# Kernel tuning notes

Hardware: AMD Instinct MI355X
Metric: run time of the kernel (lower is better)

Reference implementation:

```python
import jax, jax.numpy as jnp
import numpy as np

B, DIM, H, W = 1, 256, 64, 64
NUM_HEADS = 8
N_GROUPS = 4
KK = 9                      # ksizes[blk_ids=0]
KV_H, KV_W = 64, 64         # kv_size[blk_ids=0]
NGC = DIM // N_GROUPS       # n_group_channels = 64
NHC = DIM // NUM_HEADS      # n_head_channels = 32
NGH = NUM_HEADS // N_GROUPS # n_group_heads = 2
OFFSET_RANGE_FACTOR = 2.0
SCALE = NHC ** -0.5
LN_EPS = 1e-5


def setup_inputs() -> dict:
    key = jax.random.key(0)
    ks = jax.random.split(key, 10)
    def n(k, shape, std=0.02):
        return jax.random.normal(k, shape, jnp.float32) * std
    return {
        "x": jax.random.normal(ks[0], (B, DIM, H, W), jnp.float32),
        "wq": n(ks[1], (DIM, DIM)), "bq": jnp.zeros((DIM,), jnp.float32),
        "wk": n(ks[2], (DIM, DIM)), "bk": jnp.zeros((DIM,), jnp.float32),
        "wv": n(ks[3], (DIM, DIM)), "bv": jnp.zeros((DIM,), jnp.float32),
        "w_off_dw": n(ks[4], (NGC, 1, KK, KK)), "b_off_dw": jnp.zeros((NGC,), jnp.float32),
        "ln_g": jnp.ones((NGC,), jnp.float32), "ln_b": jnp.zeros((NGC,), jnp.float32),
        "w_off_pw": n(ks[5], (2, NGC)),
        "rpe_table": n(ks[6], (NUM_HEADS, 2 * KV_H - 1, 2 * KV_W - 1), 0.01),
        "w_out": n(ks[7], (DIM, DIM)), "b_out": jnp.zeros((DIM,), jnp.float32),
    }


def conv1x1(x, w, b=None):
    # x: [B,C,H,W], w: [O,C]
    y = jnp.einsum('bchw,oc->bohw', x, w)
    if b is not None:
        y = y + b[None, :, None, None]
    return y


def grid_sample_bilinear(inp, grid):
    # Faithful F.grid_sample(mode='bilinear', align_corners=True, padding_mode='zeros').
    # inp: [N,C,Hi,Wi], grid: [N,Hg,Wg,2] with (x,y) in [-1,1].
    N, C, Hi, Wi = inp.shape
    gx = (grid[..., 0] + 1.0) * 0.5 * (Wi - 1)
    gy = (grid[..., 1] + 1.0) * 0.5 * (Hi - 1)
    x0 = jnp.floor(gx)
    y0 = jnp.floor(gy)
    gather_b = jax.vmap(lambda im, iy, ix: im[:, iy, ix])  # -> [N,C,Hg,Wg]
    out = jnp.zeros((N, C) + grid.shape[1:3], inp.dtype)
    for dy in (0.0, 1.0):
        for dx in (0.0, 1.0):
            ix = x0 + dx
            iy = y0 + dy
            wgt = (1.0 - jnp.abs(gx - ix)) * (1.0 - jnp.abs(gy - iy))
            valid = (ix >= 0) & (ix <= Wi - 1) & (iy >= 0) & (iy <= Hi - 1)
            ixc = jnp.clip(ix, 0, Wi - 1).astype(jnp.int32)
            iyc = jnp.clip(iy, 0, Hi - 1).astype(jnp.int32)
            out = out + gather_b(inp, iyc, ixc) * (wgt * valid)[:, None]
    return out


def ref_points(Hk, Wk, n):
    # normalized (y, x) reference grid, matching _get_ref_points
    ry = (jnp.arange(Hk, dtype=jnp.float32) + 0.5) / Hk * 2.0 - 1.0
    rx = (jnp.arange(Wk, dtype=jnp.float32) + 0.5) / Wk * 2.0 - 1.0
    ref = jnp.stack(jnp.meshgrid(ry, rx, indexing='ij'), -1)  # [Hk,Wk,2]
    return jnp.broadcast_to(ref[None], (n, Hk, Wk, 2))


def reference(x, wq, bq, wk, bk, wv, bv, w_off_dw, b_off_dw, ln_g, ln_b,
              w_off_pw, rpe_table, w_out, b_out):
    Bx, C, Hx, Wx = x.shape
    q = conv1x1(x, wq, bq)
    q_off = q.reshape(Bx * N_GROUPS, NGC, Hx, Wx)

    # conv_offset: depthwise conv -> LayerNorm(channels) -> GELU -> 1x1 conv (no bias)
    o = jax.lax.conv_general_dilated(
        q_off, w_off_dw, window_strides=(1, 1),
        padding=[(KK // 2, KK // 2), (KK // 2, KK // 2)],
        feature_group_count=NGC,
        dimension_numbers=('NCHW', 'OIHW', 'NCHW'))
    o = o + b_off_dw[None, :, None, None]
    mu = o.mean(1, keepdims=True)
    var = o.var(1, keepdims=True)
    o = (o - mu) / jnp.sqrt(var + LN_EPS) * ln_g[None, :, None, None] + ln_b[None, :, None, None]
    o = jax.nn.gelu(o, approximate=False)
    offset = jnp.einsum('bchw,oc->bohw', o, w_off_pw)  # [B*g, 2, Hk, Wk]

    Hk, Wk = offset.shape[2], offset.shape[3]
    n_sample = Hk * Wk
    off_range = jnp.array([1.0 / Hk, 1.0 / Wk], jnp.float32).reshape(1, 2, 1, 1)
    offset = jnp.tanh(offset) * off_range * OFFSET_RANGE_FACTOR
    offset = offset.transpose(0, 2, 3, 1)  # [B*g, Hk, Wk, 2] (y, x)

    pos = offset + ref_points(Hk, Wk, Bx * N_GROUPS)

    x_g = x.reshape(Bx * N_GROUPS, NGC, Hx, Wx)
    x_sampled = grid_sample_bilinear(x_g, pos[..., ::-1])  # grid is (x, y)
    x_sampled = x_sampled.reshape(Bx, C, 1, n_sample)

    qf = q.reshape(Bx * NUM_HEADS, NHC, Hx * Wx)
    k = conv1x1(x_sampled, wk, bk).reshape(Bx * NUM_HEADS, NHC, n_sample)
    v = conv1x1(x_sampled, wv, bv).reshape(Bx * NUM_HEADS, NHC, n_sample)

    attn = jnp.einsum('bcm,bcn->bmn', qf, k) * SCALE  # [B*h, HW, n_sample]

    # RPE bias via bilinear sampling of rpe_table at displacement grid
    q_grid = ref_points(Hx, Wx, Bx * N_GROUPS)
    disp = (q_grid.reshape(Bx * N_GROUPS, Hx * Wx, 1, 2)
            - pos.reshape(Bx * N_GROUPS, 1, n_sample, 2)) * 0.5
    rpe = jnp.broadcast_to(rpe_table[None], (Bx,) + rpe_table.shape)
    rpe = rpe.reshape(Bx * N_GROUPS, NGH, 2 * Hx - 1, 2 * Wx - 1)
    attn_bias = grid_sample_bilinear(rpe, disp[..., ::-1])
    attn_bias = attn_bias.reshape(Bx * NUM_HEADS, Hx * Wx, n_sample)

    attn = jax.nn.softmax(attn + attn_bias, axis=2)
    out = jnp.einsum('bmn,bcn->bcm', attn, v).reshape(Bx, C, Hx, Wx)
    return conv1x1(out, w_out, b_out)
```

## Files before the change

### kernel.cpp

```cpp
#include <hip/hip_runtime.h>
#include <hip/hip_bf16.h>
#include <math.h>

#define HW 4096
#define SCALE 0.17677669529663687f
#define LOG2E 1.4426950408889634f

typedef __attribute__((ext_vector_type(8))) short short8;
typedef __attribute__((ext_vector_type(4))) float f32x4;
typedef __attribute__((ext_vector_type(4))) unsigned int u32x4;
typedef __attribute__((ext_vector_type(2))) unsigned int u32x2;
typedef __attribute__((ext_vector_type(2), aligned(8))) unsigned int u32x2a;

static __device__ __forceinline__ unsigned short bf16b(float f) {
  __hip_bfloat16 h = __float2bfloat16(f);
  return *reinterpret_cast<unsigned short*>(&h);
}

__global__ __launch_bounds__(256) void gemm256(const float* __restrict__ W,
                                               const float* __restrict__ bias,
                                               const float* __restrict__ X,
                                               float* __restrict__ Yf,
                                               unsigned short* __restrict__ Yt,
                                               float sc) {
  int tid = threadIdx.x;
  int o0 = (blockIdx.x >> 4) * 8;
  int p = (blockIdx.x & 15) * 256 + tid;
  const float* Wb = W + o0 * 256;
  float acc[8];
  #pragma unroll
  for (int i = 0; i < 8; ++i) acc[i] = 0.f;
  #pragma unroll 4
  for (int c = 0; c < 256; ++c) {
    float xv = X[c * HW + p];
    #pragma unroll
    for (int i = 0; i < 8; ++i) acc[i] += Wb[i * 256 + c] * xv;
  }
  float r[8];
  #pragma unroll
  for (int i = 0; i < 8; ++i) r[i] = acc[i] + bias[o0 + i];
  if (Yf) {
    #pragma unroll
    for (int i = 0; i < 8; ++i) Yf[(size_t)(o0 + i) * HW + p] = r[i];
  }
  if (Yt) {
    int h = o0 >> 5, c0 = o0 & 31;
    u32x4 pk;
    #pragma unroll
    for (int j = 0; j < 4; ++j)
      pk[j] = (unsigned int)bf16b(r[2 * j] * sc) | ((unsigned int)bf16b(r[2 * j + 1] * sc) << 16);
    *(u32x4*)(Yt + ((size_t)(h * HW + p) * 32 + c0)) = pk;
  }
}

__global__ __launch_bounds__(256) void gemm_kv(const float* __restrict__ Wk,
                                               const float* __restrict__ bk,
                                               const float* __restrict__ Wv,
                                               const float* __restrict__ bv,
                                               const float* __restrict__ X,
                                               unsigned short* __restrict__ Yt,
                                               unsigned short* __restrict__ Yv) {
  int tid = threadIdx.x;
  int o0 = (blockIdx.x >> 4) * 8;
  int p = (blockIdx.x & 15) * 256 + tid;
  const float* Wkb = Wk + o0 * 256;
  const float* Wvb = Wv + o0 * 256;
  float ka[8], va[8];
  #pragma unroll
  for (int i = 0; i < 8; ++i) { ka[i] = 0.f; va[i] = 0.f; }
  #pragma unroll 2
  for (int c = 0; c < 256; ++c) {
    float xv = X[c * HW + p];
    #pragma unroll
    for (int i = 0; i < 8; ++i) {
      ka[i] += Wkb[i * 256 + c] * xv;
      va[i] += Wvb[i * 256 + c] * xv;
    }
  }
  {
    int h = o0 >> 5, c0 = o0 & 31;
    u32x4 pk;
    #pragma unroll
    for (int j = 0; j < 4; ++j) {
      float k0 = ka[2 * j] + bk[o0 + 2 * j];
      float k1 = ka[2 * j + 1] + bk[o0 + 2 * j + 1];
      pk[j] = (unsigned int)bf16b(k0) | ((unsigned int)bf16b(k1) << 16);
    }
    *(u32x4*)(Yt + ((size_t)(h * HW + p) * 32 + c0)) = pk;
  }
  #pragma unroll
  for (int i = 0; i < 8; ++i)
    Yv[(size_t)(o0 + i) * HW + p] = bf16b(va[i] + bv[o0 + i]);
}

__global__ __launch_bounds__(256) void dwconv_kernel(const float* __restrict__ q,
                                                     const float* __restrict__ wdw,
                                                     const float* __restrict__ bdw,
                                                     float* __restrict__ o) {
  int x = threadIdx.x & 63;
  int w = threadIdx.x >> 6;
  int bid = blockIdx.x;
  int half = bid & 1; int c = (bid >> 1) & 63; int g = bid >> 7;
  int y0 = half * 32 + w * 8;
  const float* qc = q + (g * 64 + c) * HW;
  const float* wc = wdw + c * 81;
  float b = bdw[c];
  float acc[8];
  #pragma unroll
  for (int i = 0; i < 8; ++i) acc[i] = b;
  #pragma unroll
  for (int r = 0; r < 16; ++r) {
    int yy = y0 - 4 + r;
    bool rowok = (unsigned)yy <= 63u;
    int yc = min(max(yy, 0), 63);
    float v[9];
    #pragma unroll
    for (int kx = 0; kx < 9; ++kx) {
      int xx = x + kx - 4;
      bool ok = rowok && ((unsigned)xx <= 63u);
      int xc = min(max(xx, 0), 63);
      float lv = qc[yc * 64 + xc];
      v[kx] = ok ? lv : 0.f;
    }
    #pragma unroll
    for (int oy = 0; oy < 8; ++oy) {
      int ky = r - oy;
      if (ky < 0 || ky > 8) continue;
      #pragma unroll
      for (int kx = 0; kx < 9; ++kx)
        acc[oy] += wc[ky * 9 + kx] * v[kx];
    }
  }
  #pragma unroll
  for (int oy = 0; oy < 8; ++oy)
    o[(g * 64 + c) * HW + (y0 + oy) * 64 + x] = acc[oy];
}

__global__ __launch_bounds__(256) void ln_offset_kernel(const float* __restrict__ o,
                                                        const float* __restrict__ ln_g,
                                                        const float* __restrict__ ln_b,
                                                        const float* __restrict__ wpw,
                                                        float* __restrict__ pos,
                                                        float* __restrict__ cxy) {
  int wave = threadIdx.x >> 6;
  int c = threadIdx.x & 63;
  int bid = blockIdx.x;
  int xc = bid & 15; int y = (bid >> 4) & 63; int g = bid >> 10;
  int x = xc * 4 + wave;
  int p = y * 64 + x;
  float v = o[(g * 64 + c) * HW + p];
  float s = v, s2 = v * v;
  #pragma unroll
  for (int m = 32; m; m >>= 1) { s += __shfl_xor(s, m); s2 += __shfl_xor(s2, m); }
  float mu = s * (1.f / 64.f);
  float var = s2 * (1.f / 64.f) - mu * mu;
  float nv = (v - mu) * rsqrtf(var + 1e-5f) * ln_g[c] + ln_b[c];
  nv = 0.5f * nv * (1.f + erff(nv * 0.70710678118654752f));
  float t0 = wpw[c] * nv, t1 = wpw[64 + c] * nv;
  #pragma unroll
  for (int m = 32; m; m >>= 1) { t0 += __shfl_xor(t0, m); t1 += __shfl_xor(t1, m); }
  if (c == 0) {
    float offy = tanhf(t0) * (2.0f / 64.0f);
    float offx = tanhf(t1) * (2.0f / 64.0f);
    float py = offy + (y + 0.5f) * (2.f / 64.f) - 1.f;
    float px = offx + (x + 0.5f) * (2.f / 64.f) - 1.f;
    pos[(g * HW + p) * 2 + 0] = py;
    pos[(g * HW + p) * 2 + 1] = px;
    cxy[(g * HW + p) * 2 + 0] = 64.0f - 31.5f * px;
    cxy[(g * HW + p) * 2 + 1] = 64.0f - 31.5f * py;
  }
}

__global__ __launch_bounds__(256) void sample_kernel(const float* __restrict__ x,
                                                     const float* __restrict__ pos,
                                                     float* __restrict__ xs) {
  int bid = blockIdx.x;
  int cc = bid & 15; int nt = (bid >> 4) & 15; int g = bid >> 8;
  int n = nt * 256 + threadIdx.x;
  float py = pos[(g * HW + n) * 2 + 0];
  float px = pos[(g * HW + n) * 2 + 1];
  float gx = (px + 1.f) * 31.5f;
  float gy = (py + 1.f) * 31.5f;
  float xf = floorf(gx), yf = floorf(gy);
  int xi = (int)xf, yi = (int)yf;
  float fx = gx - xf, fy = gy - yf;
  int x0c = min(max(xi, 0), 63), x1c = min(max(xi + 1, 0), 63);
  int y0c = min(max(yi, 0), 63), y1c = min(max(yi + 1, 0), 63);
  float wx0 = ((unsigned)xi <= 63u) ? (1.f - fx) : 0.f;
  float wx1 = ((unsigned)(xi + 1) <= 63u) ? fx : 0.f;
  float wy0 = ((unsigned)yi <= 63u) ? (1.f - fy) : 0.f;
  float wy1 = ((unsigned)(yi + 1) <= 63u) ? fy : 0.f;
  #pragma unroll
  for (int ci = 0; ci < 4; ++ci) {
    int c = cc * 4 + ci;
    const float* xp = x + (g * 64 + c) * HW;
    float vsum = wy0 * (wx0 * xp[y0c * 64 + x0c] + wx1 * xp[y0c * 64 + x1c]) +
                 wy1 * (wx0 * xp[y1c * 64 + x0c] + wx1 * xp[y1c * 64 + x1c]);
    xs[(g * 64 + c) * HW + n] = vsum;
  }
}

__global__ __launch_bounds__(256) void build_rpe4_kernel(const float* __restrict__ rpe,
                                                         unsigned int* __restrict__ tab4) {
  int idx = blockIdx.x * 256 + threadIdx.x;
  if (idx >= 8 * 16641) return;
  int h = idx / 16641; int r = idx - h * 16641;
  int y = r / 129, x = r - y * 129;
  const float* tb = rpe + h * 16129;
  auto pad = [&](int yy, int xx) -> float {
    if (yy < 1 || yy > 127 || xx < 1 || xx > 127) return 0.f;
    return tb[(yy - 1) * 127 + (xx - 1)] * LOG2E;
  };
  unsigned int w0 = (unsigned int)bf16b(pad(y, x)) | ((unsigned int)bf16b(pad(y + 1, x)) << 16);
  unsigned int w1 = (unsigned int)bf16b(pad(y, x + 1)) | ((unsigned int)bf16b(pad(y + 1, x + 1)) << 16);
  u32x2 v = {w0, w1};
  *(u32x2*)(tab4 + (size_t)idx * 2) = v;
}

__global__ __launch_bounds__(256, 3) void attn_kernel(const unsigned short* __restrict__ qt,
                                                      const unsigned short* __restrict__ kt,
                                                      const unsigned short* __restrict__ vbuf,
                                                      const float* __restrict__ cxy,
                                                      const unsigned int* __restrict__ tab4,
                                                      float* __restrict__ att) {
  __shared__ __align__(16) unsigned int P_pack[4][16][20];
  __shared__ float red_l[4][16];
  __shared__ float red_acc[4][32][16];

  int tid = threadIdx.x;
  int w = tid >> 6;
  int l = tid & 63;
  int lm = l & 15;
  int lg = l >> 4;
  int h = blockIdx.x >> 8;
  int mt = blockIdx.x & 255;
  int m0 = mt * 16;
  int m = m0 + lm;
  int xm = m & 63, ym = m >> 6;
  float ex = (xm + 0.5f) * (63.0f / 64.0f) - 31.5f;
  float ey = (ym + 0.5f) * (63.0f / 64.0f) - 31.5f;
  const char* tabb = (const char*)tab4 + (size_t)h * 133128;
  const float* cbase = cxy + (size_t)(h >> 1) * HW * 2;

  short8 qf = *(const short8*)(qt + ((size_t)(h * HW + m) * 32 + 8 * lg));

  f32x4 oA = {0.f, 0.f, 0.f, 0.f};
  f32x4 oB = {0.f, 0.f, 0.f, 0.f};
  float l_lane = 0.f;

  float bias[8];
  float2 ccv[8];
  short8 ka, kb, va, vb;

  {
    float2 cc0[8];
    #pragma unroll
    for (int i = 0; i < 8; ++i) {
      int nl = 16 * (i >> 2) + 4 * lg + (i & 3);
      cc0[i] = *(const float2*)(cbase + (size_t)(w * 32 + nl) * 2);
    }
    int n0 = w * 32;
    ka = *(const short8*)(kt + ((size_t)(h * HW + n0 + lm) * 32 + 8 * lg));
    kb = *(const short8*)(kt + ((size_t)(h * HW + n0 + 16 + lm) * 32 + 8 * lg));
    va = *(const short8*)(vbuf + ((size_t)(h * 32 + lm) * HW + n0 + 8 * lg));
    vb = *(const short8*)(vbuf + ((size_t)(h * 32 + 16 + lm) * HW + n0 + 8 * lg));
    u32x2a tv[8];
    float fxs[8], fys[8];
    #pragma unroll
    for (int i = 0; i < 8; ++i) {
      float gx = ex + cc0[i].x, gy = ey + cc0[i].y;
      float xf = floorf(gx), yf = floorf(gy);
      fxs[i] = gx - xf; fys[i] = gy - yf;
      unsigned off = (unsigned)((int)yf * 1032 + ((int)xf << 3));
      tv[i] = *(const u32x2a*)(tabb + off);
    }
    #pragma unroll
    for (int i = 0; i < 8; ++i) {
      int nl = 16 * (i >> 2) + 4 * lg + (i & 3);
      ccv[i] = *(const float2*)(cbase + (size_t)(128 + w * 32 + nl) * 2);
    }
    #pragma unroll
    for (int i = 0; i < 8; ++i) {
      float a00 = __uint_as_float(tv[i][0] << 16);
      float a10 = __uint_as_float(tv[i][0] & 0xffff0000u);
      float a01 = __uint_as_float(tv[i][1] << 16);
      float a11 = __uint_as_float(tv[i][1] & 0xffff0000u);
      float ly0 = a00 + fys[i] * (a10 - a00);
      float ly1 = a01 + fys[i] * (a11 - a01);
      bias[i] = ly0 + fxs[i] * (ly1 - ly0);
    }
  }

  #pragma unroll 2
  for (int it = 0; it < 32; ++it) {
    f32x4 z = {0.f, 0.f, 0.f, 0.f};
    f32x4 s0 = __builtin_amdgcn_mfma_f32_16x16x32_bf16(ka, qf, z, 0, 0, 0);
    f32x4 s1 = __builtin_amdgcn_mfma_f32_16x16x32_bf16(kb, qf, z, 0, 0, 0);

    int n0n = ((it + 1) & 31) * 128 + w * 32;
    short8 kan = *(const short8*)(kt + ((size_t)(h * HW + n0n + lm) * 32 + 8 * lg));
    short8 kbn = *(const short8*)(kt + ((size_t)(h * HW + n0n + 16 + lm) * 32 + 8 * lg));
    short8 van = *(const short8*)(vbuf + ((size_t)(h * 32 + lm) * HW + n0n + 8 * lg));
    short8 vbn = *(const short8*)(vbuf + ((size_t)(h * 32 + 16 + lm) * HW + n0n + 8 * lg));

    u32x2a tv[8];
    float fxs[8], fys[8];
    #pragma unroll
    for (int i = 0; i < 8; ++i) {
      float gx = ex + ccv[i].x, gy = ey + ccv[i].y;
      float xf = floorf(gx), yf = floorf(gy);
      fxs[i] = gx - xf; fys[i] = gy - yf;
      unsigned off = (unsigned)((int)yf * 1032 + ((int)xf << 3));
      tv[i] = *(const u32x2a*)(tabb + off);
    }
    int n0n2 = ((it + 2) & 31) * 128 + w * 32;
    float2 ccn[8];
    #pragma unroll
    for (int i = 0; i < 8; ++i) {
      int nl = 16 * (i >> 2) + 4 * lg + (i & 3);
      ccn[i] = *(const float2*)(cbase + (size_t)(n0n2 + nl) * 2);
    }

    float p[8];
    #pragma unroll
    for (int i = 0; i < 8; ++i) {
      float qk = (i < 4) ? s0[i & 3] : s1[i & 3];
      p[i] = __builtin_amdgcn_exp2f(qk + bias[i]);
    }
    l_lane += ((p[0] + p[1]) + (p[2] + p[3])) + ((p[4] + p[5]) + (p[6] + p[7]));
    unsigned int w0 = (unsigned int)bf16b(p[0]) | ((unsigned int)bf16b(p[1]) << 16);
    unsigned int w1 = (unsigned int)bf16b(p[2]) | ((unsigned int)bf16b(p[3]) << 16);
    unsigned int w2 = (unsigned int)bf16b(p[4]) | ((unsigned int)bf16b(p[5]) << 16);
    unsigned int w3 = (unsigned int)bf16b(p[6]) | ((unsigned int)bf16b(p[7]) << 16);
    u32x2 wa = {w0, w1}, wb = {w2, w3};
    *(u32x2*)&P_pack[w][lm][2 * lg] = wa;
    *(u32x2*)&P_pack[w][lm][8 + 2 * lg] = wb;
    u32x4 pw = *(u32x4*)&P_pack[w][lm][4 * lg];
    union { u32x4 u; short8 s; } cv; cv.u = pw;
    oA = __builtin_amdgcn_mfma_f32_16x16x32_bf16(va, cv.s, oA, 0, 0, 0);
    oB = __builtin_amdgcn_mfma_f32_16x16x32_bf16(vb, cv.s, oB, 0, 0, 0);

    #pragma unroll
    for (int i = 0; i < 8; ++i) {
      float a00 = __uint_as_float(tv[i][0] << 16);
      float a10 = __uint_as_float(tv[i][0] & 0xffff0000u);
      float a01 = __uint_as_float(tv[i][1] << 16);
      float a11 = __uint_as_float(tv[i][1] & 0xffff0000u);
      float ly0 = a00 + fys[i] * (a10 - a00);
      float ly1 = a01 + fys[i] * (a11 - a01);
      bias[i] = ly0 + fxs[i] * (ly1 - ly0);
    }
    ka = kan; kb = kbn; va = van; vb = vbn;
    #pragma unroll
    for (int i = 0; i < 8; ++i) ccv[i] = ccn[i];
  }

  l_lane += __shfl_xor(l_lane, 16);
  l_lane += __shfl_xor(l_lane, 32);
  if (lg == 0) red_l[w][lm] = l_lane;
  #pragma unroll
  for (int r = 0; r < 4; ++r) {
    red_acc[w][4 * lg + r][lm] = oA[r];
    red_acc[w][16 + 4 * lg + r][lm] = oB[r];
  }
  __syncthreads();
  #pragma unroll
  for (int rep = 0; rep < 2; ++rep) {
    int idx = tid + rep * 256;
    int cl = idx >> 4, mm = idx & 15;
    float lsum = 0.f, osum = 0.f;
    #pragma unroll
    for (int ww = 0; ww < 4; ++ww) {
      lsum += red_l[ww][mm];
      osum += red_acc[ww][cl][mm];
    }
    att[(size_t)(h * 32 + cl) * HW + m0 + mm] = osum / lsum;
  }
}

extern "C" void kernel_launch(void* const* d_in, const int* in_sizes, int n_in,
                              void* d_out, int out_size, void* d_ws, size_t ws_size,
                              hipStream_t stream) {
  const float* x    = (const float*)d_in[0];
  const float* wq   = (const float*)d_in[1];
  const float* bq   = (const float*)d_in[2];
  const float* wk   = (const float*)d_in[3];
  const float* bk   = (const float*)d_in[4];
  const float* wv   = (const float*)d_in[5];
  const float* bv   = (const float*)d_in[6];
  const float* wdw  = (const float*)d_in[7];
  const float* bdw  = (const float*)d_in[8];
  const float* lng  = (const float*)d_in[9];
  const float* lnb  = (const float*)d_in[10];
  const float* wpw  = (const float*)d_in[11];
  const float* rpe  = (const float*)d_in[12];
  const float* wout = (const float*)d_in[13];
  const float* bout = (const float*)d_in[14];
  float* out = (float*)d_out;

  float* ws = (float*)d_ws;
  float* q_f32 = ws;
  float* o_f32 = ws + (1 << 20);
  unsigned short* qt  = (unsigned short*)(ws + (2 << 20));
  unsigned short* ktp = (unsigned short*)(ws + ((2 << 20) + (1 << 19)));
  unsigned short* vbp = (unsigned short*)(ws + (3 << 20));
  float* pos  = ws + ((3 << 20) + (1 << 19));
  float* cxy  = pos + 32768;
  unsigned int* tab4 = (unsigned int*)(cxy + 32768);

  gemm256<<<512, 256, 0, stream>>>(wq, bq, x, q_f32, qt, SCALE * LOG2E);
  build_rpe4_kernel<<<521, 256, 0, stream>>>(rpe, tab4);
  dwconv_kernel<<<512, 256, 0, stream>>>(q_f32, wdw, bdw, o_f32);
  ln_offset_kernel<<<4096, 256, 0, stream>>>(o_f32, lng, lnb, wpw, pos, cxy);
  sample_kernel<<<1024, 256, 0, stream>>>(x, pos, q_f32);
  gemm_kv<<<512, 256, 0, stream>>>(wk, bk, wv, bv, q_f32, ktp, vbp);
  attn_kernel<<<2048, 256, 0, stream>>>(qt, ktp, vbp, cxy, tab4, o_f32);
  gemm256<<<512, 256, 0, stream>>>(wout, bout, o_f32, out, nullptr, 1.0f);
}
```

Before: 296.8 us.

## Load RPE table entries cooperatively and redistribute via ds_bpermute

Instead of each lane gathering its own scattered RPE table entry, lanes in a 16-lane group load a contiguous run of table entries based on the group's base x position, then use ds_bpermute to fetch the needed entry by relative index. This turns random gathers into coalesced loads. It adds two cross-lane permutes per sample and assumes the per-lane x offset relative to the base stays within 0..15, which holds only if the offsets vary slowly across the row.

```diff
diff --git a/kernel.cpp b/kernel.cpp
--- a/kernel.cpp
+++ b/kernel.cpp
@@ -239,6 +239,7 @@
   int xm = m & 63, ym = m >> 6;
   float ex = (xm + 0.5f) * (63.0f / 64.0f) - 31.5f;
   float ey = (ym + 0.5f) * (63.0f / 64.0f) - 31.5f;
+  float exb = ((m0 & 63) + 0.5f) * (63.0f / 64.0f) - 31.5f;
   const char* tabb = (const char*)tab4 + (size_t)h * 133128;
   const float* cbase = cxy + (size_t)(h >> 1) * HW * 2;
 
@@ -264,15 +265,21 @@
     kb = *(const short8*)(kt + ((size_t)(h * HW + n0 + 16 + lm) * 32 + 8 * lg));
     va = *(const short8*)(vbuf + ((size_t)(h * 32 + lm) * HW + n0 + 8 * lg));
     vb = *(const short8*)(vbuf + ((size_t)(h * 32 + 16 + lm) * HW + n0 + 8 * lg));
-    u32x2a tv[8];
+    u32x2a wentry[8];
     float fxs[8], fys[8];
-    #pragma unroll
-    for (int i = 0; i < 8; ++i) {
-      float gx = ex + cc0[i].x, gy = ey + cc0[i].y;
-      float xf = floorf(gx), yf = floorf(gy);
-      fxs[i] = gx - xf; fys[i] = gy - yf;
-      unsigned off = (unsigned)((int)yf * 1032 + ((int)xf << 3));
-      tv[i] = *(const u32x2a*)(tabb + off);
+    int jidx[8];
+    #pragma unroll
+    for (int i = 0; i < 8; ++i) {
+      float gxl = ex + cc0[i].x;
+      float gyu = ey + cc0[i].y;
+      float yfu = floorf(gyu);
+      fys[i] = gyu - yfu;
+      float xbf = floorf(exb + cc0[i].x);
+      float xfl = floorf(gxl);
+      fxs[i] = gxl - xfl;
+      jidx[i] = (int)(xfl - xbf);
+      unsigned woff = (unsigned)((((int)yfu * 129 + (int)xbf + lm) << 3));
+      wentry[i] = *(const u32x2a*)(tabb + woff);
     }
     #pragma unroll
     for (int i = 0; i < 8; ++i) {
@@ -281,10 +288,13 @@
     }
     #pragma unroll
     for (int i = 0; i < 8; ++i) {
-      float a00 = __uint_as_float(tv[i][0] << 16);
-      float a10 = __uint_as_float(tv[i][0] & 0xffff0000u);
-      float a01 = __uint_as_float(tv[i][1] << 16);
-      float a11 = __uint_as_float(tv[i][1] & 0xffff0000u);
+      int srcb = ((lg << 4) + jidx[i]) << 2;
+      unsigned e0 = (unsigned)__builtin_amdgcn_ds_bpermute(srcb, (int)wentry[i][0]);
+      unsigned e1 = (unsigned)__builtin_amdgcn_ds_bpermute(srcb, (int)wentry[i][1]);
+      float a00 = __uint_as_float(e0 << 16);
+      float a10 = __uint_as_float(e0 & 0xffff0000u);
+      float a01 = __uint_as_float(e1 << 16);
+      float a11 = __uint_as_float(e1 & 0xffff0000u);
       float ly0 = a00 + fys[i] * (a10 - a00);
       float ly1 = a01 + fys[i] * (a11 - a01);
       bias[i] = ly0 + fxs[i] * (ly1 - ly0);
@@ -303,15 +313,21 @@
     short8 van = *(const short8*)(vbuf + ((size_t)(h * 32 + lm) * HW + n0n + 8 * lg));
     short8 vbn = *(const short8*)(vbuf + ((size_t)(h * 32 + 16 + lm) * HW + n0n + 8 * lg));
 
-    u32x2a tv[8];
+    u32x2a wentry[8];
     float fxs[8], fys[8];
-    #pragma unroll
-    for (int i = 0; i < 8; ++i) {
-      float gx = ex + ccv[i].x, gy = ey + ccv[i].y;
-      float xf = floorf(gx), yf = floorf(gy);
-      fxs[i] = gx - xf; fys[i] = gy - yf;
-      unsigned off = (unsigned)((int)yf * 1032 + ((int)xf << 3));
-      tv[i] = *(const u32x2a*)(tabb + off);
+    int jidx[8];
+    #pragma unroll
+    for (int i = 0; i < 8; ++i) {
+      float gxl = ex + ccv[i].x;
+      float gyu = ey + ccv[i].y;
+      float yfu = floorf(gyu);
+      fys[i] = gyu - yfu;
+      float xbf = floorf(exb + ccv[i].x);
+      float xfl = floorf(gxl);
+      fxs[i] = gxl - xfl;
+      jidx[i] = (int)(xfl - xbf);
+      unsigned woff = (unsigned)((((int)yfu * 129 + (int)xbf + lm) << 3));
+      wentry[i] = *(const u32x2a*)(tabb + woff);
     }
     int n0n2 = ((it + 2) & 31) * 128 + w * 32;
     float2 ccn[8];
@@ -342,10 +358,13 @@
 
     #pragma unroll
     for (int i = 0; i < 8; ++i) {
-      float a00 = __uint_as_float(tv[i][0] << 16);
-      float a10 = __uint_as_float(tv[i][0] & 0xffff0000u);
-      float a01 = __uint_as_float(tv[i][1] << 16);
-      float a11 = __uint_as_float(tv[i][1] & 0xffff0000u);
+      int srcb = ((lg << 4) + jidx[i]) << 2;
+      unsigned e0 = (unsigned)__builtin_amdgcn_ds_bpermute(srcb, (int)wentry[i][0]);
+      unsigned e1 = (unsigned)__builtin_amdgcn_ds_bpermute(srcb, (int)wentry[i][1]);
+      float a00 = __uint_as_float(e0 << 16);
+      float a10 = __uint_as_float(e0 & 0xffff0000u);
+      float a01 = __uint_as_float(e1 << 16);
+      float a11 = __uint_as_float(e1 & 0xffff0000u);
       float ly0 = a00 + fys[i] * (a10 - a00);
       float ly1 = a01 + fys[i] * (a11 - a01);
       bias[i] = ly0 + fxs[i] * (ly1 - ly0);
```

Result: no change. 300.3 us (+1.2%).

## Process both heads of a group per attention block to share offset work

Applied to the files above, without the earlier changes.

Each attention block now handles the two heads that share one offset group, so the sampling-position loads, floor/fraction computation and table-address math are done once and used for both heads. The grid is halved to 1024 blocks and each thread keeps two sets of K/V fragments, biases and accumulators. This trades more registers and LDS per block, and the loop is no longer unrolled by two, which may lower occupancy against the launch bound of 3 blocks per CU and reduce latency hiding.

```diff
diff --git a/kernel.cpp b/kernel.cpp
--- a/kernel.cpp
+++ b/kernel.cpp
@@ -223,34 +223,37 @@
                                                       const float* __restrict__ cxy,
                                                       const unsigned int* __restrict__ tab4,
                                                       float* __restrict__ att) {
-  __shared__ __align__(16) unsigned int P_pack[4][16][20];
-  __shared__ float red_l[4][16];
-  __shared__ float red_acc[4][32][16];
+  __shared__ __align__(16) unsigned int P_pack[2][4][16][20];
+  __shared__ float red_l[2][4][16];
+  __shared__ float red_acc[2][4][32][16];
 
   int tid = threadIdx.x;
   int w = tid >> 6;
   int l = tid & 63;
   int lm = l & 15;
   int lg = l >> 4;
-  int h = blockIdx.x >> 8;
+  int g = blockIdx.x >> 8;
   int mt = blockIdx.x & 255;
   int m0 = mt * 16;
   int m = m0 + lm;
   int xm = m & 63, ym = m >> 6;
   float ex = (xm + 0.5f) * (63.0f / 64.0f) - 31.5f;
   float ey = (ym + 0.5f) * (63.0f / 64.0f) - 31.5f;
-  const char* tabb = (const char*)tab4 + (size_t)h * 133128;
-  const float* cbase = cxy + (size_t)(h >> 1) * HW * 2;
-
-  short8 qf = *(const short8*)(qt + ((size_t)(h * HW + m) * 32 + 8 * lg));
-
-  f32x4 oA = {0.f, 0.f, 0.f, 0.f};
-  f32x4 oB = {0.f, 0.f, 0.f, 0.f};
-  float l_lane = 0.f;
-
-  float bias[8];
+  int h0 = g * 2;
+  const char* tb0 = (const char*)tab4 + (size_t)h0 * 133128;
+  const char* tb1 = tb0 + 133128;
+  const float* cbase = cxy + (size_t)g * HW * 2;
+
+  short8 qf0 = *(const short8*)(qt + ((size_t)(h0 * HW + m) * 32 + 8 * lg));
+  short8 qf1 = *(const short8*)(qt + ((size_t)((h0 + 1) * HW + m) * 32 + 8 * lg));
+
+  f32x4 o0A = {0.f, 0.f, 0.f, 0.f}, o0B = {0.f, 0.f, 0.f, 0.f};
+  f32x4 o1A = {0.f, 0.f, 0.f, 0.f}, o1B = {0.f, 0.f, 0.f, 0.f};
+  float l0 = 0.f, l1 = 0.f;
+
+  float bias0[8], bias1[8];
   float2 ccv[8];
-  short8 ka, kb, va, vb;
+  short8 k0a, k0b, v0a, v0b, k1a, k1b, v1a, v1b;
 
   {
     float2 cc0[8];
@@ -260,11 +263,15 @@
       cc0[i] = *(const float2*)(cbase + (size_t)(w * 32 + nl) * 2);
     }
     int n0 = w * 32;
-    ka = *(const short8*)(kt + ((size_t)(h * HW + n0 + lm) * 32 + 8 * lg));
-    kb = *(const short8*)(kt + ((size_t)(h * HW + n0 + 16 + lm) * 32 + 8 * lg));
-    va = *(const short8*)(vbuf + ((size_t)(h * 32 + lm) * HW + n0 + 8 * lg));
-    vb = *(const short8*)(vbuf + ((size_t)(h * 32 + 16 + lm) * HW + n0 + 8 * lg));
-    u32x2a tv[8];
+    k0a = *(const short8*)(kt + ((size_t)(h0 * HW + n0 + lm) * 32 + 8 * lg));
+    k0b = *(const short8*)(kt + ((size_t)(h0 * HW + n0 + 16 + lm) * 32 + 8 * lg));
+    v0a = *(const short8*)(vbuf + ((size_t)(h0 * 32 + lm) * HW + n0 + 8 * lg));
+    v0b = *(const short8*)(vbuf + ((size_t)(h0 * 32 + 16 + lm) * HW + n0 + 8 * lg));
+    k1a = *(const short8*)(kt + ((size_t)((h0 + 1) * HW + n0 + lm) * 32 + 8 * lg));
+    k1b = *(const short8*)(kt + ((size_t)((h0 + 1) * HW + n0 + 16 + lm) * 32 + 8 * lg));
+    v1a = *(const short8*)(vbuf + ((size_t)((h0 + 1) * 32 + lm) * HW + n0 + 8 * lg));
+    v1b = *(const short8*)(vbuf + ((size_t)((h0 + 1) * 32 + 16 + lm) * HW + n0 + 8 * lg));
+    u32x2a t0[8], t1[8];
     float fxs[8], fys[8];
     #pragma unroll
     for (int i = 0; i < 8; ++i) {
@@ -272,7 +279,8 @@
       float xf = floorf(gx), yf = floorf(gy);
       fxs[i] = gx - xf; fys[i] = gy - yf;
       unsigned off = (unsigned)((int)yf * 1032 + ((int)xf << 3));
-      tv[i] = *(const u32x2a*)(tabb + off);
+      t0[i] = *(const u32x2a*)(tb0 + off);
+      t1[i] = *(const u32x2a*)(tb1 + off);
     }
     #pragma unroll
     for (int i = 0; i < 8; ++i) {
@@ -281,29 +289,41 @@
     }
     #pragma unroll
     for (int i = 0; i < 8; ++i) {
-      float a00 = __uint_as_float(tv[i][0] << 16);
-      float a10 = __uint_as_float(tv[i][0] & 0xffff0000u);
-      float a01 = __uint_as_float(tv[i][1] << 16);
-      float a11 = __uint_as_float(tv[i][1] & 0xffff0000u);
+      float a00 = __uint_as_float(t0[i][0] << 16);
+      float a10 = __uint_as_float(t0[i][0] & 0xffff0000u);
+      float a01 = __uint_as_float(t0[i][1] << 16);
+      float a11 = __uint_as_float(t0[i][1] & 0xffff0000u);
       float ly0 = a00 + fys[i] * (a10 - a00);
       float ly1 = a01 + fys[i] * (a11 - a01);
-      bias[i] = ly0 + fxs[i] * (ly1 - ly0);
-    }
-  }
-
-  #pragma unroll 2
+      bias0[i] = ly0 + fxs[i] * (ly1 - ly0);
+      float b00 = __uint_as_float(t1[i][0] << 16);
+      float b10 = __uint_as_float(t1[i][0] & 0xffff0000u);
+      float b01 = __uint_as_float(t1[i][1] << 16);
+      float b11 = __uint_as_float(t1[i][1] & 0xffff0000u);
+      float my0 = b00 + fys[i] * (b10 - b00);
+      float my1 = b01 + fys[i] * (b11 - b01);
+      bias1[i] = my0 + fxs[i] * (my1 - my0);
+    }
+  }
+
   for (int it = 0; it < 32; ++it) {
     f32x4 z = {0.f, 0.f, 0.f, 0.f};
-    f32x4 s0 = __builtin_amdgcn_mfma_f32_16x16x32_bf16(ka, qf, z, 0, 0, 0);
-    f32x4 s1 = __builtin_amdgcn_mfma_f32_16x16x32_bf16(kb, qf, z, 0, 0, 0);
+    f32x4 s0a = __builtin_amdgcn_mfma_f32_16x16x32_bf16(k0a, qf0, z, 0, 0, 0);
+    f32x4 s0b = __builtin_amdgcn_mfma_f32_16x16x32_bf16(k0b, qf0, z, 0, 0, 0);
+    f32x4 s1a = __builtin_amdgcn_mfma_f32_16x16x32_bf16(k1a, qf1, z, 0, 0, 0);
+    f32x4 s1b = __builtin_amdgcn_mfma_f32_16x16x32_bf16(k1b, qf1, z, 0, 0, 0);
 
     int n0n = ((it + 1) & 31) * 128 + w * 32;
-    short8 kan = *(const short8*)(kt + ((size_t)(h * HW + n0n + lm) * 32 + 8 * lg));
-    short8 kbn = *(const short8*)(kt + ((size_t)(h * HW + n0n + 16 + lm) * 32 + 8 * lg));
-    short8 van = *(const short8*)(vbuf + ((size_t)(h * 32 + lm) * HW + n0n + 8 * lg));
-    short8 vbn = *(const short8*)(vbuf + ((size_t)(h * 32 + 16 + lm) * HW + n0n + 8 * lg));
-
-    u32x2a tv[8];
+    short8 k0an = *(const short8*)(kt + ((size_t)(h0 * HW + n0n + lm) * 32 + 8 * lg));
+    short8 k0bn = *(const short8*)(kt + ((size_t)(h0 * HW + n0n + 16 + lm) * 32 + 8 * lg));
+    short8 v0an = *(const short8*)(vbuf + ((size_t)(h0 * 32 + lm) * HW + n0n + 8 * lg));
+    short8 v0bn = *(const short8*)(vbuf + ((size_t)(h0 * 32 + 16 + lm) * HW + n0n + 8 * lg));
+    short8 k1an = *(const short8*)(kt + ((size_t)((h0 + 1) * HW + n0n + lm) * 32 + 8 * lg));
+    short8 k1bn = *(const short8*)(kt + ((size_t)((h0 + 1) * HW + n0n + 16 + lm) * 32 + 8 * lg));
+    short8 v1an = *(const short8*)(vbuf + ((size_t)((h0 + 1) * 32 + lm) * HW + n0n + 8 * lg));
+    short8 v1bn = *(const short8*)(vbuf + ((size_t)((h0 + 1) * 32 + 16 + lm) * HW + n0n + 8 * lg));
+
+    u32x2a t0[8], t1[8];
     float fxs[8], fys[8];
     #pragma unroll
     for (int i = 0; i < 8; ++i) {
@@ -311,7 +331,8 @@
       float xf = floorf(gx), yf = floorf(gy);
       fxs[i] = gx - xf; fys[i] = gy - yf;
       unsigned off = (unsigned)((int)yf * 1032 + ((int)xf << 3));
-      tv[i] = *(const u32x2a*)(tabb + off);
+      t0[i] = *(const u32x2a*)(tb0 + off);
+      t1[i] = *(const u32x2a*)(tb1 + off);
     }
     int n0n2 = ((it + 2) & 31) * 128 + w * 32;
     float2 ccn[8];
@@ -321,60 +342,90 @@
       ccn[i] = *(const float2*)(cbase + (size_t)(n0n2 + nl) * 2);
     }
 
-    float p[8];
-    #pragma unroll
-    for (int i = 0; i < 8; ++i) {
-      float qk = (i < 4) ? s0[i & 3] : s1[i & 3];
-      p[i] = __builtin_amdgcn_exp2f(qk + bias[i]);
-    }
-    l_lane += ((p[0] + p[1]) + (p[2] + p[3])) + ((p[4] + p[5]) + (p[6] + p[7]));
-    unsigned int w0 = (unsigned int)bf16b(p[0]) | ((unsigned int)bf16b(p[1]) << 16);
-    unsigned int w1 = (unsigned int)bf16b(p[2]) | ((unsigned int)bf16b(p[3]) << 16);
-    unsigned int w2 = (unsigned int)bf16b(p[4]) | ((unsigned int)bf16b(p[5]) << 16);
-    unsigned int w3 = (unsigned int)bf16b(p[6]) | ((unsigned int)bf16b(p[7]) << 16);
-    u32x2 wa = {w0, w1}, wb = {w2, w3};
-    *(u32x2*)&P_pack[w][lm][2 * lg] = wa;
-    *(u32x2*)&P_pack[w][lm][8 + 2 * lg] = wb;
-    u32x4 pw = *(u32x4*)&P_pack[w][lm][4 * lg];
-    union { u32x4 u; short8 s; } cv; cv.u = pw;
-    oA = __builtin_amdgcn_mfma_f32_16x16x32_bf16(va, cv.s, oA, 0, 0, 0);
-    oB = __builtin_amdgcn_mfma_f32_16x16x32_bf16(vb, cv.s, oB, 0, 0, 0);
-
-    #pragma unroll
-    for (int i = 0; i < 8; ++i) {
-      float a00 = __uint_as_float(tv[i][0] << 16);
-      float a10 = __uint_as_float(tv[i][0] & 0xffff0000u);
-      float a01 = __uint_as_float(tv[i][1] << 16);
-      float a11 = __uint_as_float(tv[i][1] & 0xffff0000u);
+    float p0[8], p1[8];
+    #pragma unroll
+    for (int i = 0; i < 8; ++i) {
+      float q0 = (i < 4) ? s0a[i & 3] : s0b[i & 3];
+      float q1 = (i < 4) ? s1a[i & 3] : s1b[i & 3];
+      p0[i] = __builtin_amdgcn_exp2f(q0 + bias0[i]);
+      p1[i] = __builtin_amdgcn_exp2f(q1 + bias1[i]);
+    }
+    l0 += ((p0[0] + p0[1]) + (p0[2] + p0[3])) + ((p0[4] + p0[5]) + (p0[6] + p0[7]));
+    l1 += ((p1[0] + p1[1]) + (p1[2] + p1[3])) + ((p1[4] + p1[5]) + (p1[6] + p1[7]));
+    {
+      unsigned int w0 = (unsigned int)bf16b(p0[0]) | ((unsigned int)bf16b(p0[1]) << 16);
+      unsigned int w1 = (unsigned int)bf16b(p0[2]) | ((unsigned int)bf16b(p0[3]) << 16);
+      unsigned int w2 = (unsigned int)bf16b(p0[4]) | ((unsigned int)bf16b(p0[5]) << 16);
+      unsigned int w3 = (unsigned int)bf16b(p0[6]) | ((unsigned int)bf16b(p0[7]) << 16);
+      u32x2 wa = {w0, w1}, wb = {w2, w3};
+      *(u32x2*)&P_pack[0][w][lm][2 * lg] = wa;
+      *(u32x2*)&P_pack[0][w][lm][8 + 2 * lg] = wb;
+    }
+    {
+      unsigned int w0 = (unsigned int)bf16b(p1[0]) | ((unsigned int)bf16b(p1[1]) << 16);
+      unsigned int w1 = (unsigned int)bf16b(p1[2]) | ((unsigned int)bf16b(p1[3]) << 16);
+      unsigned int w2 = (unsigned int)bf16b(p1[4]) | ((unsigned int)bf16b(p1[5]) << 16);
+      unsigned int w3 = (unsigned int)bf16b(p1[6]) | ((unsigned int)bf16b(p1[7]) << 16);
+      u32x2 wa = {w0, w1}, wb = {w2, w3};
+      *(u32x2*)&P_pack[1][w][lm][2 * lg] = wa;
+      *(u32x2*)&P_pack[1][w][lm][8 + 2 * lg] = wb;
+    }
+    {
+      u32x4 pw0 = *(u32x4*)&P_pack[0][w][lm][4 * lg];
+      union { u32x4 u; short8 s; } c0; c0.u = pw0;
+      o0A = __builtin_amdgcn_mfma_f32_16x16x32_bf16(v0a, c0.s, o0A, 0, 0, 0);
+      o0B = __builtin_amdgcn_mfma_f32_16x16x32_bf16(v0b, c0.s, o0B, 0, 0, 0);
+      u32x4 pw1 = *(u32x4*)&P_pack[1][w][lm][4 * lg];
+      union { u32x4 u; short8 s; } c1; c1.u = pw1;
+      o1A = __builtin_amdgcn_mfma_f32_16x16x32_bf16(v1a, c1.s, o1A, 0, 0, 0);
+      o1B = __builtin_amdgcn_mfma_f32_16x16x32_bf16(v1b, c1.s, o1B, 0, 0, 0);
+    }
+
+    #pragma unroll
+    for (int i = 0; i < 8; ++i) {
+      float a00 = __uint_as_float(t0[i][0] << 16);
+      float a10 = __uint_as_float(t0[i][0] & 0xffff0000u);
+      float a01 = __uint_as_float(t0[i][1] << 16);
+      float a11 = __uint_as_float(t0[i][1] & 0xffff0000u);
       float ly0 = a00 + fys[i] * (a10 - a00);
       float ly1 = a01 + fys[i] * (a11 - a01);
-      bias[i] = ly0 + fxs[i] * (ly1 - ly0);
-    }
-    ka = kan; kb = kbn; va = van; vb = vbn;
+      bias0[i] = ly0 + fxs[i] * (ly1 - ly0);
+      float b00 = __uint_as_float(t1[i][0] << 16);
+      float b10 = __uint_as_float(t1[i][0] & 0xffff0000u);
+      float b01 = __uint_as_float(t1[i][1] << 16);
+      float b11 = __uint_as_float(t1[i][1] & 0xffff0000u);
+      float my0 = b00 + fys[i] * (b10 - b00);
+      float my1 = b01 + fys[i] * (b11 - b01);
+      bias1[i] = my0 + fxs[i] * (my1 - my0);
+    }
+    k0a = k0an; k0b = k0bn; v0a = v0an; v0b = v0bn;
+    k1a = k1an; k1b = k1bn; v1a = v1an; v1b = v1bn;
     #pragma unroll
     for (int i = 0; i < 8; ++i) ccv[i] = ccn[i];
   }
 
-  l_lane += __shfl_xor(l_lane, 16);
-  l_lane += __shfl_xor(l_lane, 32);
-  if (lg == 0) red_l[w][lm] = l_lane;
+  l0 += __shfl_xor(l0, 16); l0 += __shfl_xor(l0, 32);
+  l1 += __shfl_xor(l1, 16); l1 += __shfl_xor(l1, 32);
+  if (lg == 0) { red_l[0][w][lm] = l0; red_l[1][w][lm] = l1; }
   #pragma unroll
   for (int r = 0; r < 4; ++r) {
-    red_acc[w][4 * lg + r][lm] = oA[r];
-    red_acc[w][16 + 4 * lg + r][lm] = oB[r];
+    red_acc[0][w][4 * lg + r][lm] = o0A[r];
+    red_acc[0][w][16 + 4 * lg + r][lm] = o0B[r];
+    red_acc[1][w][4 * lg + r][lm] = o1A[r];
+    red_acc[1][w][16 + 4 * lg + r][lm] = o1B[r];
   }
   __syncthreads();
   #pragma unroll
-  for (int rep = 0; rep < 2; ++rep) {
+  for (int rep = 0; rep < 8; ++rep) {
     int idx = tid + rep * 256;
-    int cl = idx >> 4, mm = idx & 15;
+    int hh = idx >> 10, cl = (idx >> 4) & 31, mm = idx & 15;
     float lsum = 0.f, osum = 0.f;
     #pragma unroll
     for (int ww = 0; ww < 4; ++ww) {
-      lsum += red_l[ww][mm];
-      osum += red_acc[ww][cl][mm];
-    }
-    att[(size_t)(h * 32 + cl) * HW + m0 + mm] = osum / lsum;
+      lsum += red_l[hh][ww][mm];
+      osum += red_acc[hh][ww][cl][mm];
+    }
+    att[(size_t)((h0 + hh) * 32 + cl) * HW + m0 + mm] = osum / lsum;
   }
 }
 
@@ -414,6 +465,6 @@
   ln_offset_kernel<<<4096, 256, 0, stream>>>(o_f32, lng, lnb, wpw, pos, cxy);
   sample_kernel<<<1024, 256, 0, stream>>>(x, pos, q_f32);
   gemm_kv<<<512, 256, 0, stream>>>(wk, bk, wv, bv, q_f32, ktp, vbp);
-  attn_kernel<<<2048, 256, 0, stream>>>(qt, ktp, vbp, cxy, tab4, o_f32);
+  attn_kernel<<<1024, 256, 0, stream>>>(qt, ktp, vbp, cxy, tab4, o_f32);
   gemm256<<<512, 256, 0, stream>>>(wout, bout, o_f32, out, nullptr, 1.0f);
 }
```

Result: no change. 293.7 us (-1.1%).
